# Kernel optimization log

Hardware: AMD Instinct MI355X
Metric: run time of the kernel (lower is better)

## Reference

```python
import jax, jax.numpy as jnp
import numpy as np
import math

B, S, D_MODEL, H, D_LATENT = 2, 2048, 2048, 16, 512
D_HEAD = D_MODEL // H


def setup_inputs() -> dict:
    key = jax.random.key(0)
    ks = jax.random.split(key, 6)
    s = lambda fan: 1.0 / math.sqrt(fan)
    return {
        "x": jax.random.normal(ks[0], (B, S, D_MODEL), dtype=jnp.float32),
        "W_q": jax.random.normal(ks[1], (D_MODEL, D_MODEL), dtype=jnp.float32) * s(D_MODEL),
        "W_down_kv": jax.random.normal(ks[2], (D_LATENT, D_MODEL), dtype=jnp.float32) * s(D_MODEL),
        "W_up_k": jax.random.normal(ks[3], (H, D_HEAD, D_LATENT), dtype=jnp.float32) * s(D_LATENT),
        "W_up_v": jax.random.normal(ks[4], (H, D_HEAD, D_LATENT), dtype=jnp.float32) * s(D_LATENT),
        "W_o": jax.random.normal(ks[5], (D_MODEL, D_MODEL), dtype=jnp.float32) * s(D_MODEL),
    }


def reference(x, W_q, W_down_kv, W_up_k, W_up_v, W_o):
    b, s_len, d_model = x.shape
    # Q: (B, H, S, Dh)
    Q = (x @ W_q.T).reshape(b, s_len, H, D_HEAD).transpose(0, 2, 1, 3)
    # latent KV: (B, S, d_latent)
    C_kv = x @ W_down_kv.T
    # per-head up-projections fused into one einsum: (B, H, S, Dh)
    K = jnp.einsum("bsl,hdl->bhsd", C_kv, W_up_k)
    V = jnp.einsum("bsl,hdl->bhsd", C_kv, W_up_v)
    scores = jnp.einsum("bhsd,bhtd->bhst", Q, K) / math.sqrt(D_HEAD)
    attn = jax.nn.softmax(scores, axis=-1)  # dropout p=0 / eval -> identity
    out = jnp.einsum("bhst,bhtd->bhsd", attn, V)
    out = out.transpose(0, 2, 1, 3).reshape(b, s_len, H * D_HEAD)
    return out @ W_o.T
```

## Files before the change

kernel.cpp:

```cpp
#include <hip/hip_runtime.h>
#include <hip/hip_bf16.h>

typedef __hip_bfloat16 bf16;
typedef __attribute__((ext_vector_type(8))) short short8v;
typedef __attribute__((ext_vector_type(4))) short short4v;
typedef __attribute__((ext_vector_type(4))) float f32x4;

#define MFMA_16x16x32(a, b, c) __builtin_amdgcn_mfma_f32_16x16x32_bf16((a), (b), (c), 0, 0, 0)

constexpr int Bc = 2, Sc = 2048, DMc = 2048, Hc = 16, DLc = 512, DHc = 128;

__device__ __forceinline__ void gload_lds16(const bf16* g, void* lds) {
  __builtin_amdgcn_global_load_lds(
      (const __attribute__((address_space(1))) void*)g,
      (__attribute__((address_space(3))) void*)lds, 16, 0, 0);
}

__device__ __forceinline__ unsigned short bf16bits(float f) {
  return __builtin_bit_cast(unsigned short, __float2bfloat16(f));
}

struct CvtArgs {
  const float* src[6];
  bf16* dst[6];
  unsigned int cum[6];
  unsigned int total4;
};

__global__ __launch_bounds__(256) void cvt_all_kernel(CvtArgs a)
{
  unsigned int i = blockIdx.x * 256 + threadIdx.x;
  const unsigned int stride = gridDim.x * 256;
  for (; i < a.total4; i += stride) {
    int s = 0;
#pragma unroll
    for (int k = 1; k < 6; ++k) s += (i >= a.cum[k]) ? 1 : 0;
    unsigned int off = (i - a.cum[s]) * 4;
    float4 v = *(const float4*)(a.src[s] + off);
    short4v p;
    p[0] = (short)bf16bits(v.x);
    p[1] = (short)bf16bits(v.y);
    p[2] = (short)bf16bits(v.z);
    p[3] = (short)bf16bits(v.w);
    *(short4v*)(a.dst[s] + off) = p;
  }
}

template<int EPI>
__device__ __forceinline__ void gemm_tile_128(
    const bf16* __restrict__ A, const bf16* __restrict__ BT, void* __restrict__ Cv,
    int K, int ldc, int row0, int col0, bf16* As, bf16* Bs)
{
  const int tid = threadIdx.x;
  const int lane = tid & 63, wid = tid >> 6;
  const int wr = wid >> 1, wc = wid & 1;

  f32x4 acc[4][4] = {};

  const int srow = tid >> 2;
  const int scol = (tid & 3) * 8;
  const bf16* Ag = A + (size_t)(row0 + srow) * K + scol;
  const bf16* Bg = BT + (size_t)(col0 + srow) * K + scol;
  char* AsW = (char*)As + wid * 1024;
  char* BsW = (char*)Bs + wid * 1024;

  const int fr = lane & 15, fk = (lane >> 4) * 8;
  const bf16* aRd = As + (wr * 64 + fr) * 32 + fk;
  const bf16* bRd = Bs + (wc * 64 + fr) * 32 + fk;

  for (int k0 = 0; k0 < K; k0 += 32) {
    gload_lds16(Ag, AsW);
    gload_lds16(Ag + (size_t)64 * K, AsW + 4096);
    gload_lds16(Bg, BsW);
    gload_lds16(Bg + (size_t)64 * K, BsW + 4096);
    Ag += 32; Bg += 32;
    __syncthreads();
    short8v a[4], b[4];
#pragma unroll
    for (int m = 0; m < 4; ++m) a[m] = *(const short8v*)(aRd + m * 16 * 32);
#pragma unroll
    for (int n = 0; n < 4; ++n) b[n] = *(const short8v*)(bRd + n * 16 * 32);
#pragma unroll
    for (int m = 0; m < 4; ++m)
#pragma unroll
      for (int n = 0; n < 4; ++n)
        acc[m][n] = MFMA_16x16x32(a[m], b[n], acc[m][n]);
    __syncthreads();
  }

  const int crow = (lane >> 4) * 4, ccol = lane & 15;
  if (EPI == 0) {
    bf16* C = (bf16*)Cv;
#pragma unroll
    for (int m = 0; m < 4; ++m)
#pragma unroll
      for (int n = 0; n < 4; ++n) {
        bf16* Cp = C + (size_t)(row0 + wr * 64 + m * 16 + crow) * ldc
                     + col0 + wc * 64 + n * 16 + ccol;
#pragma unroll
        for (int r = 0; r < 4; ++r)
          Cp[(size_t)r * ldc] = __float2bfloat16(acc[m][n][r]);
      }
  } else if (EPI == 1) {
    bf16* C = (bf16*)Cv;
#pragma unroll
    for (int m = 0; m < 4; ++m)
#pragma unroll
      for (int n = 0; n < 4; ++n) {
        short4v pk;
#pragma unroll
        for (int r = 0; r < 4; ++r)
          pk[r] = (short)bf16bits(acc[m][n][r]);
        bf16* Cp = C + (size_t)(col0 + wc * 64 + n * 16 + ccol) * ldc
                     + row0 + wr * 64 + m * 16 + crow;
        *(short4v*)Cp = pk;
      }
  } else {
    float* C = (float*)Cv;
#pragma unroll
    for (int m = 0; m < 4; ++m)
#pragma unroll
      for (int n = 0; n < 4; ++n) {
        float* Cp = C + (size_t)(row0 + wr * 64 + m * 16 + crow) * ldc
                      + col0 + wc * 64 + n * 16 + ccol;
#pragma unroll
        for (int r = 0; r < 4; ++r)
          Cp[(size_t)r * ldc] = acc[m][n][r];
      }
  }
}

template<int EPI>
__global__ __launch_bounds__(256) void gemm_bt_kernel(
    const bf16* __restrict__ A, const bf16* __restrict__ BT, void* __restrict__ C,
    int K, int N)
{
  __shared__ bf16 As[128 * 32];
  __shared__ bf16 Bs[128 * 32];
  gemm_tile_128<EPI>(A, BT, C, K, N, blockIdx.y * 128, blockIdx.x * 128, As, Bs);
}

__global__ __launch_bounds__(256) void qkv_gemm_kernel(
    const bf16* __restrict__ xb, const bf16* __restrict__ Wqb,
    const bf16* __restrict__ Wdkvb, bf16* __restrict__ Qb, bf16* __restrict__ Ck)
{
  __shared__ bf16 As[128 * 32];
  __shared__ bf16 Bs[128 * 32];
  const int bx = blockIdx.x, row0 = blockIdx.y * 128;
  if (bx < 16)
    gemm_tile_128<0>(xb, Wqb, Qb, DMc, DMc, row0, bx * 128, As, Bs);
  else
    gemm_tile_128<0>(xb, Wdkvb, Ck, DMc, DLc, row0, (bx - 16) * 128, As, Bs);
}

__global__ __launch_bounds__(256) void up_gemm_kernel(
    const bf16* __restrict__ Ck, const bf16* __restrict__ Wukb,
    const bf16* __restrict__ Wuvb, bf16* __restrict__ Kcat, bf16* __restrict__ VTcat)
{
  __shared__ bf16 As[128 * 32];
  __shared__ bf16 Bs[128 * 32];
  const int bx = blockIdx.x, row0 = blockIdx.y * 128;
  if (bx < 16)
    gemm_tile_128<0>(Ck, Wukb, Kcat, DLc, DMc, row0, bx * 128, As, Bs);
  else
    gemm_tile_128<1>(Ck, Wuvb, VTcat, DLc, Bc * Sc, row0, (bx - 16) * 128, As, Bs);
}

constexpr int KVB = 64;
constexpr int NTT = Sc / KVB;
constexpr int VSTR = Bc * Sc;

__global__ __launch_bounds__(512, 2) void mla_attn_kernel(
    const bf16* __restrict__ Q, const bf16* __restrict__ Kcat,
    const bf16* __restrict__ VTcat, bf16* __restrict__ O)
{
  __shared__ bf16 Ks[2][KVB * DHc];
  __shared__ bf16 Vs[2][DHc * KVB];
  __shared__ bf16 Pl[8 * 2 * 1024];

  const int tid = threadIdx.x, lane = tid & 63, wid = tid >> 6;
  const int h = blockIdx.y, b = blockIdx.z;
  const int q0 = blockIdx.x * 256 + wid * 32;
  const int fr = lane & 15, fg = lane >> 4;

  const bf16* Qp = Q + (size_t)(b * Sc + q0 + fr) * DMc + h * DHc + fg * 8;
  short8v qf[2][4];
#pragma unroll
  for (int mi = 0; mi < 2; ++mi)
#pragma unroll
    for (int kf = 0; kf < 4; ++kf)
      qf[mi][kf] = *(const short8v*)(Qp + (size_t)mi * 16 * DMc + kf * 32);

  const bf16* Kb = Kcat + (size_t)b * Sc * DMc + h * DHc;
  const bf16* Vb = VTcat + (size_t)(h * DHc) * VSTR + b * Sc;

  const int krow = wid * 4 + fg;
  const int kcolB = (fr * 16) ^ ((krow & 7) << 4);
  const bf16* kp = Kb + (size_t)krow * DMc + (kcolB >> 1);
  const int vrow = wid * 8 + (lane >> 3);
  const int vcolB = ((lane & 7) * 16) ^ ((lane >> 3) << 4);
  const bf16* vp = Vb + (size_t)vrow * VSTR + (vcolB >> 1);

  auto STAGE = [&](int buf) {
    char* kd = (char*)(&Ks[buf][0]) + wid * 1024;
    gload_lds16(kp, kd);
    gload_lds16(kp + (size_t)32 * DMc, kd + 8192);
    char* vd = (char*)(&Vs[buf][0]) + wid * 1024;
    gload_lds16(vp, vd);
    gload_lds16(vp + (size_t)64 * VSTR, vd + 8192);
    kp += (size_t)KVB * DMc;
    vp += KVB;
  };

  f32x4 oacc[2][8] = {};
  float m_r[2], l_r[2], msc[2];
#pragma unroll
  for (int mi = 0; mi < 2; ++mi) { m_r[mi] = -1e30f; l_r[mi] = 0.f; msc[mi] = 0.f; }
  const float SCL2 = 0.12751650f;
  const float THRraw = 47.0f;

  STAGE(0);
  int cur = 0;
  char* Pb = (char*)Pl + wid * 4096;
  const int swz = (fr & 7) << 4;

  for (int it = 0; it < NTT; ++it) {
    asm volatile("s_waitcnt vmcnt(0)" ::: "memory");
    __builtin_amdgcn_s_barrier();
    asm volatile("" ::: "memory");
    if (it + 1 < NTT) STAGE(cur ^ 1);
    asm volatile("" ::: "memory");

    f32x4 sacc[2][4] = {};
    __builtin_amdgcn_s_setprio(1);
#pragma unroll
    for (int nf = 0; nf < 4; ++nf) {
#pragma unroll
      for (int kf = 0; kf < 4; ++kf) {
        const bf16* kr = &Ks[cur][(nf * 16 + fr) * 128 +
                                  (((kf * 64 + fg * 16) ^ ((fr & 7) << 4)) >> 1)];
        short8v kfrag = *(const short8v*)kr;
        sacc[0][nf] = MFMA_16x16x32(kfrag, qf[0][kf], sacc[0][nf]);
        sacc[1][nf] = MFMA_16x16x32(kfrag, qf[1][kf], sacc[1][nf]);
      }
    }
    __builtin_amdgcn_s_setprio(0);

    float pml[2];
    float dmax = -1e30f;
#pragma unroll
    for (int mi = 0; mi < 2; ++mi) {
      float pm = sacc[mi][0][0];
#pragma unroll
      for (int nf = 0; nf < 4; ++nf)
#pragma unroll
        for (int r = 0; r < 4; ++r)
          pm = fmaxf(pm, sacc[mi][nf][r]);
      pml[mi] = pm;
      dmax = fmaxf(dmax, pm - m_r[mi]);
    }

    if (!__all(dmax <= THRraw)) {
#pragma unroll
      for (int mi = 0; mi < 2; ++mi) {
        float red = pml[mi];
        red = fmaxf(red, __shfl_xor(red, 16, 64));
        red = fmaxf(red, __shfl_xor(red, 32, 64));
        float mnew = fmaxf(m_r[mi], red);
        float c = exp2f((m_r[mi] - mnew) * SCL2);
        m_r[mi] = mnew;
        msc[mi] = mnew * SCL2;
        l_r[mi] *= c;
        f32x4 cv;
#pragma unroll
        for (int r = 0; r < 4; ++r) cv[r] = __shfl(c, fg * 4 + r, 64);
#pragma unroll
        for (int df = 0; df < 8; ++df) oacc[mi][df] *= cv;
      }
    }

#pragma unroll
    for (int mi = 0; mi < 2; ++mi) {
      char* Pm = Pb + mi * 2048;
#pragma unroll
      for (int nf = 0; nf < 4; ++nf) {
        float p0 = exp2f(__builtin_fmaf(sacc[mi][nf][0], SCL2, -msc[mi]));
        float p1 = exp2f(__builtin_fmaf(sacc[mi][nf][1], SCL2, -msc[mi]));
        float p2 = exp2f(__builtin_fmaf(sacc[mi][nf][2], SCL2, -msc[mi]));
        float p3 = exp2f(__builtin_fmaf(sacc[mi][nf][3], SCL2, -msc[mi]));
        l_r[mi] += (p0 + p1) + (p2 + p3);
        uint2 w;
        w.x = (unsigned)bf16bits(p0) | ((unsigned)bf16bits(p1) << 16);
        w.y = (unsigned)bf16bits(p2) | ((unsigned)bf16bits(p3) << 16);
        *(uint2*)(Pm + fr * 128 + ((nf * 32 + fg * 8) ^ swz)) = w;
      }
    }

    asm volatile("s_waitcnt lgkmcnt(0)" ::: "memory");
    __builtin_amdgcn_sched_barrier(0);

    short8v pa[2][2];
#pragma unroll
    for (int mi = 0; mi < 2; ++mi)
#pragma unroll
      for (int tf = 0; tf < 2; ++tf)
        pa[mi][tf] = *(const short8v*)(Pb + mi * 2048 + fr * 128 +
                                       ((tf * 64 + fg * 16) ^ swz));
    __builtin_amdgcn_sched_barrier(0);

    __builtin_amdgcn_s_setprio(1);
#pragma unroll
    for (int tf = 0; tf < 2; ++tf) {
#pragma unroll
      for (int df = 0; df < 8; ++df) {
        const bf16* vr = &Vs[cur][(df * 16 + fr) * 64 +
                                  (((tf * 64 + fg * 16) ^ ((fr & 7) << 4)) >> 1)];
        short8v vfrag = *(const short8v*)vr;
        oacc[0][df] = MFMA_16x16x32(pa[0][tf], vfrag, oacc[0][df]);
        oacc[1][df] = MFMA_16x16x32(pa[1][tf], vfrag, oacc[1][df]);
      }
    }
    __builtin_amdgcn_s_setprio(0);

    cur ^= 1;
  }

#pragma unroll
  for (int mi = 0; mi < 2; ++mi) {
    float l = l_r[mi];
    l += __shfl_xor(l, 16, 64);
    l += __shfl_xor(l, 32, 64);
    float inv = 1.f / l;
    f32x4 iv;
#pragma unroll
    for (int r = 0; r < 4; ++r) iv[r] = __shfl(inv, fg * 4 + r, 64);
    bf16* Op = O + (size_t)(b * Sc + q0 + mi * 16 + fg * 4) * DMc + h * DHc + fr;
#pragma unroll
    for (int df = 0; df < 8; ++df)
#pragma unroll
      for (int r = 0; r < 4; ++r)
        Op[(size_t)r * DMc + df * 16] = __float2bfloat16(oacc[mi][df][r] * iv[r]);
  }
}

extern "C" void kernel_launch(void* const* d_in, const int* in_sizes, int n_in,
                              void* d_out, int out_size, void* d_ws, size_t ws_size,
                              hipStream_t stream)
{
  const float* x    = (const float*)d_in[0];
  const float* Wq   = (const float*)d_in[1];
  const float* Wdkv = (const float*)d_in[2];
  const float* Wuk  = (const float*)d_in[3];
  const float* Wuv  = (const float*)d_in[4];
  const float* Wo   = (const float*)d_in[5];
  float* out = (float*)d_out;

  char* ws = (char*)d_ws;
  bf16* Qb    = (bf16*)(ws + 0);
  bf16* Kcat  = (bf16*)(ws + 16777216);
  bf16* VTcat = (bf16*)(ws + 33554432);
  bf16* xb    = (bf16*)(ws + 50331648);
  bf16* AO    = (bf16*)(ws + 50331648);
  bf16* Ck    = (bf16*)(ws + 67108864);
  bf16* Wqb   = (bf16*)(ws + 71303168);
  bf16* Wdkvb = (bf16*)(ws + 79691776);
  bf16* Wukb  = (bf16*)(ws + 81788928);
  bf16* Wuvb  = (bf16*)(ws + 83886080);
  bf16* Wob   = (bf16*)(ws + 85983232);

  dim3 blk(256, 1, 1);

  CvtArgs ca;
  ca.src[0] = x;    ca.dst[0] = xb;
  ca.src[1] = Wq;   ca.dst[1] = Wqb;
  ca.src[2] = Wdkv; ca.dst[2] = Wdkvb;
  ca.src[3] = Wuk;  ca.dst[3] = Wukb;
  ca.src[4] = Wuv;  ca.dst[4] = Wuvb;
  ca.src[5] = Wo;   ca.dst[5] = Wob;
  unsigned int n4[6] = { (unsigned)(Bc * Sc * DMc / 4), (unsigned)(DMc * DMc / 4),
                         (unsigned)(DLc * DMc / 4),     (unsigned)(Hc * DHc * DLc / 4),
                         (unsigned)(Hc * DHc * DLc / 4),(unsigned)(DMc * DMc / 4) };
  unsigned int acc = 0;
  for (int i = 0; i < 6; ++i) { ca.cum[i] = acc; acc += n4[i]; }
  ca.total4 = acc;
  cvt_all_kernel<<<2048, blk, 0, stream>>>(ca);

  qkv_gemm_kernel<<<dim3(20, (Bc * Sc) / 128), blk, 0, stream>>>(xb, Wqb, Wdkvb, Qb, Ck);

  up_gemm_kernel<<<dim3(32, (Bc * Sc) / 128), blk, 0, stream>>>(Ck, Wukb, Wuvb, Kcat, VTcat);

  mla_attn_kernel<<<dim3(Sc / 256, Hc, Bc), dim3(512, 1, 1), 0, stream>>>(
      Qb, Kcat, VTcat, AO);

  gemm_bt_kernel<2><<<dim3(DMc / 128, (Bc * Sc) / 128), blk, 0, stream>>>(AO, Wob, out, DMc, DMc);
}
```

Baseline: 258.0 us.

## Switch attention to 32x32 MFMA with register-resident P and XCD block remap

The attention kernel now uses 32x32x16 MFMA tiles, computing S transposed so each lane holds a full query row. This lets the softmax row max and row sum be reduced with a single cross-half shuffle. P is packed to bf16 with v_cvt_pk_bf16_f32 and rearranged with v_permlane32_swap, so the LDS round-trip for P and its waitcnt are gone. The K and V LDS layouts and swizzles are rebuilt to match the new fragment shapes. All GEMM kernels and the attention grid also remap block IDs so neighbouring tiles land on the same XCD for L2 reuse, at the cost of depending on hardware-specific lane semantics and fixed grid sizes.

```diff
diff --git a/kernel.cpp b/kernel.cpp
--- a/kernel.cpp
+++ b/kernel.cpp
@@ -5,8 +5,12 @@
 typedef __attribute__((ext_vector_type(8))) short short8v;
 typedef __attribute__((ext_vector_type(4))) short short4v;
 typedef __attribute__((ext_vector_type(4))) float f32x4;
+typedef __attribute__((ext_vector_type(16))) float f32x16;
+typedef __attribute__((ext_vector_type(4))) unsigned int uint4v;
+typedef unsigned int u32;
 
 #define MFMA_16x16x32(a, b, c) __builtin_amdgcn_mfma_f32_16x16x32_bf16((a), (b), (c), 0, 0, 0)
+#define MFMA_32x32x16(a, b, c) __builtin_amdgcn_mfma_f32_32x32x16_bf16((a), (b), (c), 0, 0, 0)
 
 constexpr int Bc = 2, Sc = 2048, DMc = 2048, Hc = 16, DLc = 512, DHc = 128;
 
@@ -130,6 +134,13 @@
   }
 }
 
+__device__ __forceinline__ int2 xcd_remap(int nx, int ny) {
+  int flat = blockIdx.x + nx * blockIdx.y;
+  int chunk = (nx * ny) >> 3;
+  int role = (flat & 7) * chunk + (flat >> 3);
+  return make_int2(role % nx, role / nx);
+}
+
 template<int EPI>
 __global__ __launch_bounds__(256) void gemm_bt_kernel(
     const bf16* __restrict__ A, const bf16* __restrict__ BT, void* __restrict__ C,
@@ -137,7 +148,8 @@
 {
   __shared__ bf16 As[128 * 32];
   __shared__ bf16 Bs[128 * 32];
-  gemm_tile_128<EPI>(A, BT, C, K, N, blockIdx.y * 128, blockIdx.x * 128, As, Bs);
+  int2 bb = xcd_remap(gridDim.x, gridDim.y);
+  gemm_tile_128<EPI>(A, BT, C, K, N, bb.y * 128, bb.x * 128, As, Bs);
 }
 
 __global__ __launch_bounds__(256) void qkv_gemm_kernel(
@@ -146,7 +158,8 @@
 {
   __shared__ bf16 As[128 * 32];
   __shared__ bf16 Bs[128 * 32];
-  const int bx = blockIdx.x, row0 = blockIdx.y * 128;
+  int2 bb = xcd_remap(20, 32);
+  const int bx = bb.x, row0 = bb.y * 128;
   if (bx < 16)
     gemm_tile_128<0>(xb, Wqb, Qb, DMc, DMc, row0, bx * 128, As, Bs);
   else
@@ -159,7 +172,8 @@
 {
   __shared__ bf16 As[128 * 32];
   __shared__ bf16 Bs[128 * 32];
-  const int bx = blockIdx.x, row0 = blockIdx.y * 128;
+  int2 bb = xcd_remap(32, 32);
+  const int bx = bb.x, row0 = bb.y * 128;
   if (bx < 16)
     gemm_tile_128<0>(Ck, Wukb, Kcat, DLc, DMc, row0, bx * 128, As, Bs);
   else
@@ -174,150 +188,130 @@
     const bf16* __restrict__ Q, const bf16* __restrict__ Kcat,
     const bf16* __restrict__ VTcat, bf16* __restrict__ O)
 {
-  __shared__ bf16 Ks[2][KVB * DHc];
-  __shared__ bf16 Vs[2][DHc * KVB];
-  __shared__ bf16 Pl[8 * 2 * 1024];
+  __shared__ bf16 Ks[2][KVB * 128];
+  __shared__ bf16 Vs[2][64 * 128];
 
   const int tid = threadIdx.x, lane = tid & 63, wid = tid >> 6;
-  const int h = blockIdx.y, b = blockIdx.z;
-  const int q0 = blockIdx.x * 256 + wid * 32;
-  const int fr = lane & 15, fg = lane >> 4;
-
-  const bf16* Qp = Q + (size_t)(b * Sc + q0 + fr) * DMc + h * DHc + fg * 8;
-  short8v qf[2][4];
-#pragma unroll
-  for (int mi = 0; mi < 2; ++mi)
-#pragma unroll
-    for (int kf = 0; kf < 4; ++kf)
-      qf[mi][kf] = *(const short8v*)(Qp + (size_t)mi * 16 * DMc + kf * 32);
+  const int l31 = lane & 31, hi = lane >> 5;
+
+  const int flat = blockIdx.x + 8 * (blockIdx.y + 16 * blockIdx.z);
+  const int role = (flat & 7) * 32 + (flat >> 3);
+  const int qb = role & 7, h = (role >> 3) & 15, b = role >> 7;
+  const int q0 = qb * 256 + wid * 32;
+
+  const bf16* Qp = Q + (size_t)(b * Sc + q0 + l31) * DMc + h * DHc + hi * 8;
+  short8v qf[8];
+#pragma unroll
+  for (int kk = 0; kk < 8; ++kk) qf[kk] = *(const short8v*)(Qp + kk * 16);
 
   const bf16* Kb = Kcat + (size_t)b * Sc * DMc + h * DHc;
   const bf16* Vb = VTcat + (size_t)(h * DHc) * VSTR + b * Sc;
 
-  const int krow = wid * 4 + fg;
-  const int kcolB = (fr * 16) ^ ((krow & 7) << 4);
-  const bf16* kp = Kb + (size_t)krow * DMc + (kcolB >> 1);
-  const int vrow = wid * 8 + (lane >> 3);
-  const int vcolB = ((lane & 7) * 16) ^ ((lane >> 3) << 4);
-  const bf16* vp = Vb + (size_t)vrow * VSTR + (vcolB >> 1);
-
-  auto STAGE = [&](int buf) {
+  const int srow = tid >> 4;
+  const int scol = (tid & 15) * 16;
+  const int swzKs = ((srow & 7) << 4) ^ (((srow >> 3) & 1) << 6) ^ (((srow >> 4) & 1) << 7);
+  const bf16* kp = Kb + (size_t)srow * DMc + (((scol ^ swzKs) & 255) >> 1);
+  const int swzVs = ((srow & 7) << 4) ^ (((srow >> 3) & 1) << 7);
+  const int vcp = scol ^ swzVs;
+  const bf16* vp = Vb + (size_t)(2 * srow + (vcp >> 7)) * VSTR + ((vcp & 127) >> 1);
+
+  auto STAGE = [&](int buf, int t0) {
     char* kd = (char*)(&Ks[buf][0]) + wid * 1024;
-    gload_lds16(kp, kd);
-    gload_lds16(kp + (size_t)32 * DMc, kd + 8192);
+    const bf16* k0 = kp + (size_t)t0 * DMc;
+    gload_lds16(k0, kd);
+    gload_lds16(k0 + (size_t)32 * DMc, kd + 8192);
     char* vd = (char*)(&Vs[buf][0]) + wid * 1024;
-    gload_lds16(vp, vd);
-    gload_lds16(vp + (size_t)64 * VSTR, vd + 8192);
-    kp += (size_t)KVB * DMc;
-    vp += KVB;
+    const bf16* v0 = vp + t0;
+    gload_lds16(v0, vd);
+    gload_lds16(v0 + (size_t)64 * VSTR, vd + 8192);
   };
 
-  f32x4 oacc[2][8] = {};
-  float m_r[2], l_r[2], msc[2];
-#pragma unroll
-  for (int mi = 0; mi < 2; ++mi) { m_r[mi] = -1e30f; l_r[mi] = 0.f; msc[mi] = 0.f; }
+  const int swzR = ((l31 & 7) << 4) ^ (((l31 >> 3) & 1) << 6) ^ (((l31 >> 4) & 1) << 7);
+  const int swzVR = (((l31 >> 1) & 7) << 4) ^ (((l31 >> 4) & 1) << 7);
+
+  f32x16 oacc[4] = {};
+  float m_r = -1e30f, l_r = 0.f, msc = 0.f;
   const float SCL2 = 0.12751650f;
   const float THRraw = 47.0f;
 
-  STAGE(0);
+  STAGE(0, 0);
   int cur = 0;
-  char* Pb = (char*)Pl + wid * 4096;
-  const int swz = (fr & 7) << 4;
 
   for (int it = 0; it < NTT; ++it) {
     asm volatile("s_waitcnt vmcnt(0)" ::: "memory");
     __builtin_amdgcn_s_barrier();
     asm volatile("" ::: "memory");
-    if (it + 1 < NTT) STAGE(cur ^ 1);
+    if (it + 1 < NTT) STAGE(cur ^ 1, (it + 1) * KVB);
     asm volatile("" ::: "memory");
 
-    f32x4 sacc[2][4] = {};
+    f32x16 s0 = {}, s1 = {};
+    const char* Kc = (const char*)(&Ks[cur][0]);
     __builtin_amdgcn_s_setprio(1);
 #pragma unroll
-    for (int nf = 0; nf < 4; ++nf) {
-#pragma unroll
-      for (int kf = 0; kf < 4; ++kf) {
-        const bf16* kr = &Ks[cur][(nf * 16 + fr) * 128 +
-                                  (((kf * 64 + fg * 16) ^ ((fr & 7) << 4)) >> 1)];
-        short8v kfrag = *(const short8v*)kr;
-        sacc[0][nf] = MFMA_16x16x32(kfrag, qf[0][kf], sacc[0][nf]);
-        sacc[1][nf] = MFMA_16x16x32(kfrag, qf[1][kf], sacc[1][nf]);
-      }
+    for (int kk = 0; kk < 8; ++kk) {
+      const int cb = (kk * 32 + hi * 16) ^ swzR;
+      short8v k0 = *(const short8v*)(Kc + l31 * 256 + cb);
+      short8v k1 = *(const short8v*)(Kc + (32 + l31) * 256 + cb);
+      s0 = MFMA_32x32x16(k0, qf[kk], s0);
+      s1 = MFMA_32x32x16(k1, qf[kk], s1);
     }
     __builtin_amdgcn_s_setprio(0);
 
-    float pml[2];
-    float dmax = -1e30f;
-#pragma unroll
-    for (int mi = 0; mi < 2; ++mi) {
-      float pm = sacc[mi][0][0];
-#pragma unroll
-      for (int nf = 0; nf < 4; ++nf)
-#pragma unroll
-        for (int r = 0; r < 4; ++r)
-          pm = fmaxf(pm, sacc[mi][nf][r]);
-      pml[mi] = pm;
-      dmax = fmaxf(dmax, pm - m_r[mi]);
-    }
-
-    if (!__all(dmax <= THRraw)) {
-#pragma unroll
-      for (int mi = 0; mi < 2; ++mi) {
-        float red = pml[mi];
-        red = fmaxf(red, __shfl_xor(red, 16, 64));
-        red = fmaxf(red, __shfl_xor(red, 32, 64));
-        float mnew = fmaxf(m_r[mi], red);
-        float c = exp2f((m_r[mi] - mnew) * SCL2);
-        m_r[mi] = mnew;
-        msc[mi] = mnew * SCL2;
-        l_r[mi] *= c;
-        f32x4 cv;
-#pragma unroll
-        for (int r = 0; r < 4; ++r) cv[r] = __shfl(c, fg * 4 + r, 64);
-#pragma unroll
-        for (int df = 0; df < 8; ++df) oacc[mi][df] *= cv;
-      }
-    }
-
-#pragma unroll
-    for (int mi = 0; mi < 2; ++mi) {
-      char* Pm = Pb + mi * 2048;
-#pragma unroll
-      for (int nf = 0; nf < 4; ++nf) {
-        float p0 = exp2f(__builtin_fmaf(sacc[mi][nf][0], SCL2, -msc[mi]));
-        float p1 = exp2f(__builtin_fmaf(sacc[mi][nf][1], SCL2, -msc[mi]));
-        float p2 = exp2f(__builtin_fmaf(sacc[mi][nf][2], SCL2, -msc[mi]));
-        float p3 = exp2f(__builtin_fmaf(sacc[mi][nf][3], SCL2, -msc[mi]));
-        l_r[mi] += (p0 + p1) + (p2 + p3);
-        uint2 w;
-        w.x = (unsigned)bf16bits(p0) | ((unsigned)bf16bits(p1) << 16);
-        w.y = (unsigned)bf16bits(p2) | ((unsigned)bf16bits(p3) << 16);
-        *(uint2*)(Pm + fr * 128 + ((nf * 32 + fg * 8) ^ swz)) = w;
-      }
-    }
-
-    asm volatile("s_waitcnt lgkmcnt(0)" ::: "memory");
-    __builtin_amdgcn_sched_barrier(0);
-
-    short8v pa[2][2];
-#pragma unroll
-    for (int mi = 0; mi < 2; ++mi)
-#pragma unroll
-      for (int tf = 0; tf < 2; ++tf)
-        pa[mi][tf] = *(const short8v*)(Pb + mi * 2048 + fr * 128 +
-                                       ((tf * 64 + fg * 16) ^ swz));
-    __builtin_amdgcn_sched_barrier(0);
-
+    float pm = s0[0];
+#pragma unroll
+    for (int i = 1; i < 16; ++i) pm = fmaxf(pm, s0[i]);
+#pragma unroll
+    for (int i = 0; i < 16; ++i) pm = fmaxf(pm, s1[i]);
+
+    if (!__all(pm - m_r <= THRraw)) {
+      float red = fmaxf(pm, __shfl_xor(pm, 32, 64));
+      float mnew = fmaxf(m_r, red);
+      float c = exp2f((m_r - mnew) * SCL2);
+      m_r = mnew;
+      msc = mnew * SCL2;
+      l_r *= c;
+#pragma unroll
+      for (int db = 0; db < 4; ++db) oacc[db] *= c;
+    }
+
+    short8v pf[4];
+#pragma unroll
+    for (int tt = 0; tt < 2; ++tt) {
+      const f32x16& s = tt ? s1 : s0;
+#pragma unroll
+      for (int half = 0; half < 2; ++half) {
+        float e0 = exp2f(__builtin_fmaf(s[half * 8 + 0], SCL2, -msc));
+        float e1 = exp2f(__builtin_fmaf(s[half * 8 + 1], SCL2, -msc));
+        float e2 = exp2f(__builtin_fmaf(s[half * 8 + 2], SCL2, -msc));
+        float e3 = exp2f(__builtin_fmaf(s[half * 8 + 3], SCL2, -msc));
+        float e4 = exp2f(__builtin_fmaf(s[half * 8 + 4], SCL2, -msc));
+        float e5 = exp2f(__builtin_fmaf(s[half * 8 + 5], SCL2, -msc));
+        float e6 = exp2f(__builtin_fmaf(s[half * 8 + 6], SCL2, -msc));
+        float e7 = exp2f(__builtin_fmaf(s[half * 8 + 7], SCL2, -msc));
+        l_r += ((e0 + e1) + (e2 + e3)) + ((e4 + e5) + (e6 + e7));
+        u32 cA, cB, cC, cD;
+        asm("v_cvt_pk_bf16_f32 %0, %1, %2" : "=v"(cA) : "v"(e0), "v"(e1));
+        asm("v_cvt_pk_bf16_f32 %0, %1, %2" : "=v"(cB) : "v"(e2), "v"(e3));
+        asm("v_cvt_pk_bf16_f32 %0, %1, %2" : "=v"(cC) : "v"(e4), "v"(e5));
+        asm("v_cvt_pk_bf16_f32 %0, %1, %2" : "=v"(cD) : "v"(e6), "v"(e7));
+        asm volatile("v_permlane32_swap_b32 %0, %1" : "+v"(cA), "+v"(cC));
+        asm volatile("v_permlane32_swap_b32 %0, %1" : "+v"(cB), "+v"(cD));
+        uint4v w;
+        w[0] = cA; w[1] = cB; w[2] = cC; w[3] = cD;
+        pf[tt * 2 + half] = __builtin_bit_cast(short8v, w);
+      }
+    }
+
+    const char* Vc = (const char*)(&Vs[cur][0]);
     __builtin_amdgcn_s_setprio(1);
 #pragma unroll
-    for (int tf = 0; tf < 2; ++tf) {
-#pragma unroll
-      for (int df = 0; df < 8; ++df) {
-        const bf16* vr = &Vs[cur][(df * 16 + fr) * 64 +
-                                  (((tf * 64 + fg * 16) ^ ((fr & 7) << 4)) >> 1)];
-        short8v vfrag = *(const short8v*)vr;
-        oacc[0][df] = MFMA_16x16x32(pa[0][tf], vfrag, oacc[0][df]);
-        oacc[1][df] = MFMA_16x16x32(pa[1][tf], vfrag, oacc[1][df]);
+    for (int db = 0; db < 4; ++db) {
+      const int vrow = (db * 16 + (l31 >> 1)) * 256;
+#pragma unroll
+      for (int ts = 0; ts < 4; ++ts) {
+        const int cb = ((l31 & 1) * 128 + ts * 32 + hi * 16) ^ swzVR;
+        short8v vf = *(const short8v*)(Vc + vrow + cb);
+        oacc[db] = MFMA_32x32x16(vf, pf[ts], oacc[db]);
       }
     }
     __builtin_amdgcn_s_setprio(0);
@@ -325,21 +319,19 @@
     cur ^= 1;
   }
 
-#pragma unroll
-  for (int mi = 0; mi < 2; ++mi) {
-    float l = l_r[mi];
-    l += __shfl_xor(l, 16, 64);
-    l += __shfl_xor(l, 32, 64);
-    float inv = 1.f / l;
-    f32x4 iv;
-#pragma unroll
-    for (int r = 0; r < 4; ++r) iv[r] = __shfl(inv, fg * 4 + r, 64);
-    bf16* Op = O + (size_t)(b * Sc + q0 + mi * 16 + fg * 4) * DMc + h * DHc + fr;
-#pragma unroll
-    for (int df = 0; df < 8; ++df)
+  float l = l_r + __shfl_xor(l_r, 32, 64);
+  float inv = 1.f / l;
+  bf16* Op = O + (size_t)(b * Sc + q0 + l31) * DMc + h * DHc + hi * 4;
+#pragma unroll
+  for (int db = 0; db < 4; ++db) {
+#pragma unroll
+    for (int rq = 0; rq < 4; ++rq) {
+      short4v pk;
 #pragma unroll
       for (int r = 0; r < 4; ++r)
-        Op[(size_t)r * DMc + df * 16] = __float2bfloat16(oacc[mi][df][r] * iv[r]);
+        pk[r] = (short)bf16bits(oacc[db][rq * 4 + r] * inv);
+      *(short4v*)(Op + db * 32 + rq * 8) = pk;
+    }
   }
 }
 
```

Measured after the change: 250.1 us. 3.1% less time.
